# Performance work log

Measured on AMD Instinct MI355X. Metric: run time of the kernel, lower is better.

The kernel has to match this reference:

```python
import jax, jax.numpy as jnp
import numpy as np

FCM_ITERS = 3
FCM_M = 2.0
EPS = 1e-8


def batched_index_select(x, idx):
    # x: [B, C, M, 1], idx: [B, N, K] -> [B, C, N, K]
    xt = x[..., 0]  # [B, C, M]
    return jnp.take_along_axis(xt[:, :, None, :], idx[:, None, :, :], axis=3)


def fcm_centroids(x, num_clusters):
    # Fuzzy c-means soft clustering (HyperedgeConstruction).
    # x: [B, C, N, 1] -> centroids [B, C, K], weights [B, N, 1, K]
    xt = jnp.transpose(x[..., 0], (0, 2, 1))  # [B, N, C]
    B, N, C = xt.shape
    init_idx = jnp.linspace(0, N - 1, num_clusters).astype(jnp.int32)
    cent = xt[:, init_idx, :]  # [B, K, C] deterministic init
    expo = -1.0 / (FCM_M - 1.0)

    def memberships(cent):
        xn = jnp.sum(xt * xt, axis=-1)            # [B, N]
        cn = jnp.sum(cent * cent, axis=-1)        # [B, K]
        d2 = xn[:, :, None] + cn[:, None, :] - 2.0 * jnp.einsum('bnc,bkc->bnk', xt, cent)
        d2 = jnp.maximum(d2, EPS)
        inv = d2 ** expo
        return inv / jnp.sum(inv, axis=-1, keepdims=True)  # [B, N, K]

    for _ in range(FCM_ITERS):
        u = memberships(cent)
        um = u ** FCM_M
        cent = jnp.einsum('bnk,bnc->bkc', um, xt) / (jnp.sum(um, axis=1)[..., None] + EPS)
    u = memberships(cent)
    centroids = jnp.transpose(cent, (0, 2, 1))  # [B, C, K]
    return centroids, u[:, :, None, :]          # weights [B, N, 1, K]


def setup_inputs() -> dict:
    key = jax.random.key(0)
    k1, k2, k3, k4 = jax.random.split(key, 4)
    B, C, N, K = 4, 64, 8192, 16
    OC = 64
    return {
        "x": jax.random.normal(k1, (B, C, N, 1), jnp.float32),
        "edge_index": jax.random.randint(k2, (2, B, N, K), 0, N),
        "W": jax.random.normal(k3, (OC, 3 * C), jnp.float32) / np.sqrt(3 * C).astype(np.float32),
        "b": jax.random.normal(k4, (OC,), jnp.float32) * 0.01,
        "num_clusters": 50,
        "top_clusters": 5,
    }


def reference(x, edge_index, W, b, num_clusters, top_clusters):
    B, C, N, _ = x.shape
    # max-relative neighbor feature
    x_i = batched_index_select(x, edge_index[1])          # [B, C, N, K]
    x_j = batched_index_select(x, edge_index[0])          # [B, C, N, K]
    x_j = jnp.max(x_j - x_i, axis=-1, keepdims=True)      # [B, C, N, 1]
    # soft-cluster (hyperedge) feature
    centroids, weights = fcm_centroids(x, num_clusters)   # [B,C,K], [B,N,1,K]
    weights = weights[:, :, 0, :]                         # squeeze(-2) -> [B, N, K]
    _, nn_idx_centroid = jax.lax.top_k(weights, top_clusters)  # [B, N, top]
    x_j_cluster = batched_index_select(centroids[..., None], nn_idx_centroid)  # [B, C, N, top]
    # x gathered at center_idx == x broadcast over top dim
    x_j_cluster = jnp.max(x_j_cluster - x, axis=-1, keepdims=True)  # [B, C, N, 1]
    # interleaved concat: [B, C, 3, N, 1] -> [B, 3C, N, 1]
    feat = jnp.stack([x, x_j, x_j_cluster], axis=2).reshape(B, 3 * C, N, 1)
    # BasicConv: 1x1 conv + ReLU
    out = jnp.einsum('oc,bcni->boni', W, feat) + b[None, :, None, None]
    return jax.nn.relu(out)
```

## Files before the change

### kernel.cpp

```cpp
#include <hip/hip_runtime.h>


constexpr int B  = 4;
constexpr int C  = 64;
constexpr int N  = 8192;
constexpr int KE = 16;
constexpr int OC = 64;
constexpr int NC = 50;
constexpr int TC = 5;
constexpr int C3 = 192;
constexpr int NCP = 52;
constexpr int KG  = 5;
constexpr int NKG = 10;
constexpr int NS  = 8;
constexpr int MW  = 16;
constexpr float FEPS = 1e-8f;

__global__ __launch_bounds__(256) void k_transpose(const float* __restrict__ x,
                                                   float* __restrict__ xt,
                                                   float* __restrict__ xn) {
  __shared__ float tile[64][65];
  int b  = blockIdx.x >> 7;
  int n0 = (blockIdx.x & 127) << 6;
  int tid = threadIdx.x;
  int nl = tid & 63, cq = tid >> 6;
#pragma unroll
  for (int r = 0; r < 16; ++r) {
    int cc = r * 4 + cq;
    tile[cc][nl] = x[((size_t)b * C + cc) * N + n0 + nl];
  }
  __syncthreads();
  int cl = tid & 63, nq = tid >> 6;
#pragma unroll
  for (int r = 0; r < 16; ++r) {
    int nr = r * 4 + nq;
    xt[((size_t)b * N + n0 + nr) * C + cl] = tile[cl][nr];
  }
  if (tid < 64) {
    float s = 0.f;
#pragma unroll
    for (int cc = 0; cc < 64; ++cc) { float v = tile[cc][tid]; s = fmaf(v, v, s); }
    xn[(size_t)b * N + n0 + tid] = s;
  }
}

__global__ __launch_bounds__(256) void k_init(const float* __restrict__ xt,
                                              float* __restrict__ cent,
                                              float* __restrict__ cn) {
  int i = blockIdx.x * 256 + threadIdx.x;
  int lane = threadIdx.x & 63;
  int ccol = i & 63;
  int row  = i >> 6;
  int k = row % NC, b = row / NC;
  int src = (k * (N - 1)) / (NC - 1);
  float v = xt[((size_t)b * N + src) * C + ccol];
  cent[i] = v;
  float sq = v * v;
#pragma unroll
  for (int off = 32; off; off >>= 1) sq += __shfl_down(sq, off, 64);
  if (lane == 0) cn[row] = sq;
}

__global__ __launch_bounds__(512) void k_m1(const float* __restrict__ xt,
                                            const float* __restrict__ xn,
                                            const float* __restrict__ cent,
                                            const float* __restrict__ cn,
                                            float* __restrict__ um) {
  int gid = blockIdx.x;
  int xcd = gid & 7;
  int b = xcd >> 1;
  int chunk = ((gid >> 3) << 1) + (xcd & 1);
  int n0 = chunk << 6;
  int w = __builtin_amdgcn_readfirstlane((int)threadIdx.x >> 6);
  int lane = threadIdx.x & 63;
  int n = n0 + lane;
  int base = (w < 2) ? 7 * w : 14 + 6 * (w - 2);
  int cnt  = (w < 2) ? 7 : 6;
  const float* xr = xt + ((size_t)b * N + n) * C;
  const float* cb = cent + b * NC * C;
  float dot[7];
#pragma unroll
  for (int j = 0; j < 7; ++j) dot[j] = 0.f;
  for (int c4 = 0; c4 < C; c4 += 4) {
    float4 xv = *(const float4*)(xr + c4);
#pragma unroll
    for (int j = 0; j < 7; ++j) {
      int kk = base + j; kk = (kk < NC) ? kk : 0;
      float4 cv = *(const float4*)(cb + kk * C + c4);
      dot[j] = fmaf(xv.x, cv.x, dot[j]);
      dot[j] = fmaf(xv.y, cv.y, dot[j]);
      dot[j] = fmaf(xv.z, cv.z, dot[j]);
      dot[j] = fmaf(xv.w, cv.w, dot[j]);
    }
  }
  float xnv = xn[(size_t)b * N + n];
  const float* cnb = cn + b * NC;
  float inv[7];
  float psum = 0.f;
#pragma unroll
  for (int j = 0; j < 7; ++j) {
    int kk = base + j; kk = (kk < NC) ? kk : 0;
    float d2 = fmaf(-2.f, dot[j], xnv + cnb[kk]);
    d2 = fmaxf(d2, FEPS);
    float iv = 1.f / d2;
    inv[j] = iv;
    psum += (j < cnt) ? iv : 0.f;
  }
  __shared__ float s_ps[8][64];
  s_ps[w][lane] = psum;
  __syncthreads();
  float ssum = 0.f;
#pragma unroll
  for (int ww = 0; ww < 8; ++ww) ssum += s_ps[ww][lane];
  float s2i = 1.f / (ssum * ssum);
  float* up = um + ((size_t)b * N + n) * NCP + base;
#pragma unroll
  for (int j = 0; j < 7; ++j)
    if (j < cnt) up[j] = inv[j] * inv[j] * s2i;
}

__global__ __launch_bounds__(1024) void k_m2(const float* __restrict__ um,
                                             const float* __restrict__ xt,
                                             float* __restrict__ part_c,
                                             float* __restrict__ part_u) {
  int gid = blockIdx.x;
  int xcd = gid & 7;
  int b = xcd >> 1;
  int r = ((gid >> 3) << 1) + (xcd & 1);
  int kg = r >> 3;
  int s  = r & 7;
  int k0 = kg * KG;
  int w = __builtin_amdgcn_readfirstlane((int)threadIdx.x >> 6);
  int c = threadIdx.x & 63;
  int n0 = s * (N / NS);
  const float* umb = um + ((size_t)b * N + n0) * NCP + k0;
  const float* xb  = xt + ((size_t)b * N + n0) * C + c;
  float acc[KG], ua[KG];
#pragma unroll
  for (int j = 0; j < KG; ++j) { acc[j] = 0.f; ua[j] = 0.f; }
#pragma unroll 4
  for (int n = w; n < N / NS; n += MW) {
    float xv = xb[(size_t)n * C];
    const float* up = umb + (size_t)n * NCP;
#pragma unroll
    for (int j = 0; j < KG; ++j) {
      float u = up[j];
      acc[j] = fmaf(u, xv, acc[j]);
      ua[j] += u;
    }
  }
  __shared__ float s_acc[MW][KG][64];
  __shared__ float s_ua[MW][KG];
#pragma unroll
  for (int j = 0; j < KG; ++j) s_acc[w][j][c] = acc[j];
  if (c == 0) {
#pragma unroll
    for (int j = 0; j < KG; ++j) s_ua[w][j] = ua[j];
  }
  __syncthreads();
  if (w == 0) {
#pragma unroll
    for (int j = 0; j < KG; ++j) {
      float t = 0.f;
#pragma unroll
      for (int ww = 0; ww < MW; ++ww) t += s_acc[ww][j][c];
      part_c[((size_t)s * (B * NC) + b * NC + k0 + j) * C + c] = t;
    }
    if (c == 0) {
#pragma unroll
      for (int j = 0; j < KG; ++j) {
        float t = 0.f;
#pragma unroll
        for (int ww = 0; ww < MW; ++ww) t += s_ua[ww][j];
        part_u[(size_t)s * (B * NC) + b * NC + k0 + j] = t;
      }
    }
  }
}

__global__ __launch_bounds__(256) void k_m3(const float* __restrict__ part_c,
                                            const float* __restrict__ part_u,
                                            float* __restrict__ cent,
                                            float* __restrict__ cn) {
  int i = blockIdx.x * 256 + threadIdx.x;
  int lane = threadIdx.x & 63;
  int row = i >> 6;
  float tot = 0.f;
#pragma unroll
  for (int s = 0; s < NS; ++s) tot += part_c[(size_t)s * (B * NC * C) + i];
  float us = 0.f;
#pragma unroll
  for (int s = 0; s < NS; ++s) us += part_u[(size_t)s * (B * NC) + row];
  float v = tot / (us + FEPS);
  cent[i] = v;
  float sq = v * v;
#pragma unroll
  for (int off = 32; off; off >>= 1) sq += __shfl_down(sq, off, 64);
  if (lane == 0) cn[row] = sq;
}

__global__ __launch_bounds__(512) void k_top5(const float* __restrict__ xt,
                                              const float* __restrict__ xn,
                                              const float* __restrict__ cent,
                                              const float* __restrict__ cn,
                                              int* __restrict__ t5) {
  int gid = blockIdx.x;
  int xcd = gid & 7;
  int b = xcd >> 1;
  int chunk = ((gid >> 3) << 1) + (xcd & 1);
  int n0 = chunk << 6;
  int w = __builtin_amdgcn_readfirstlane((int)threadIdx.x >> 6);
  int lane = threadIdx.x & 63;
  int n = n0 + lane;
  int base = (w < 2) ? 7 * w : 14 + 6 * (w - 2);
  int cnt  = (w < 2) ? 7 : 6;
  const float* xr = xt + ((size_t)b * N + n) * C;
  const float* cb = cent + b * NC * C;
  float dot[7];
#pragma unroll
  for (int j = 0; j < 7; ++j) dot[j] = 0.f;
  for (int c4 = 0; c4 < C; c4 += 4) {
    float4 xv = *(const float4*)(xr + c4);
#pragma unroll
    for (int j = 0; j < 7; ++j) {
      int kk = base + j; kk = (kk < NC) ? kk : 0;
      float4 cv = *(const float4*)(cb + kk * C + c4);
      dot[j] = fmaf(xv.x, cv.x, dot[j]);
      dot[j] = fmaf(xv.y, cv.y, dot[j]);
      dot[j] = fmaf(xv.z, cv.z, dot[j]);
      dot[j] = fmaf(xv.w, cv.w, dot[j]);
    }
  }
  float xnv = xn[(size_t)b * N + n];
  const float* cnb = cn + b * NC;
  __shared__ float s_inv[NC][65];
#pragma unroll
  for (int j = 0; j < 7; ++j) {
    int kk = base + j; kk = (kk < NC) ? kk : 0;
    float d2 = fmaxf(fmaf(-2.f, dot[j], xnv + cnb[kk]), FEPS);
    float iv = 1.f / d2;
    if (j < cnt) s_inv[base + j][lane] = iv;
  }
  __syncthreads();
  if (w == 0) {
    float v[NC];
#pragma unroll
    for (int k = 0; k < NC; ++k) v[k] = s_inv[k][lane];
    unsigned long long taken = 0ull;
    int* tp = t5 + ((size_t)b * N + n) * TC;
#pragma unroll
    for (int t = 0; t < TC; ++t) {
      float best = -1.f;
      int bi = 0;
#pragma unroll
      for (int k = 0; k < NC; ++k) {
        bool ok = (((taken >> k) & 1ull) == 0ull) && (v[k] > best);
        best = ok ? v[k] : best;
        bi   = ok ? k : bi;
      }
      taken |= (1ull << bi);
      tp[t] = bi;
    }
  }
}

__global__ __launch_bounds__(512, 4) void k_out(const float* __restrict__ xt,
                                                const float* __restrict__ cent,
                                                const float* __restrict__ W,
                                                const int* __restrict__ t5,
                                                const int* __restrict__ eidx,
                                                const float* __restrict__ bias,
                                                float* __restrict__ out) {
  __shared__ float s_w[OC][C3 + 2];
  int tid = threadIdx.x;
  for (int i = tid; i < OC * C3; i += 512) {
    int o = i / C3, cc = i - o * C3;
    s_w[o][cc] = W[i];
  }
  __syncthreads();
  int gid = blockIdx.x;
  int xcd = gid & 7;
  int b = xcd >> 1;
  int chunk = ((gid >> 3) << 1) + (xcd & 1);
  int wv = __builtin_amdgcn_readfirstlane(tid >> 6);
  int lane = tid & 63;
  int n0 = chunk * 64 + wv * 8;
  const float* xtb = xt + ((size_t)b * N) * C;
  const float* cb  = cent + b * NC * C;
  const int* e0b = eidx + ((size_t)b * N) * KE;
  const int* e1b = eidx + ((size_t)(B + b) * N) * KE;
  int c = lane;
  float fA[8], fB[8], fC[8];
#pragma unroll
  for (int j = 0; j < 8; ++j) {
    int n = n0 + j;
    const int* p0 = e0b + (size_t)n * KE;
    const int* p1 = e1b + (size_t)n * KE;
    const int* tp = t5 + ((size_t)b * N + n) * TC;
    float x0 = xtb[(size_t)n * C + c];
    float g0[KE], g1[KE];
#pragma unroll
    for (int k = 0; k < KE; ++k) {
      g0[k] = xtb[(size_t)p0[k] * C + c];
      g1[k] = xtb[(size_t)p1[k] * C + c];
    }
    float cv[TC];
#pragma unroll
    for (int t = 0; t < TC; ++t) cv[t] = cb[(size_t)tp[t] * C + c];
    float m1 = g0[0] - g1[0];
#pragma unroll
    for (int k = 1; k < KE; ++k) m1 = fmaxf(m1, g0[k] - g1[k]);
    float cm = cv[0];
#pragma unroll
    for (int t = 1; t < TC; ++t) cm = fmaxf(cm, cv[t]);
    fA[j] = x0; fB[j] = m1; fC[j] = cm - x0;
  }
  float bo = bias[lane];
  float acc[8];
#pragma unroll
  for (int j = 0; j < 8; ++j) acc[j] = bo;
  for (int cp = 0; cp < 64; ++cp) {
    float w0 = s_w[lane][3 * cp + 0];
    float w1 = s_w[lane][3 * cp + 1];
    float w2 = s_w[lane][3 * cp + 2];
#pragma unroll
    for (int j = 0; j < 8; ++j) {
      float a0 = __uint_as_float(__builtin_amdgcn_readlane(__float_as_uint(fA[j]), cp));
      float a1 = __uint_as_float(__builtin_amdgcn_readlane(__float_as_uint(fB[j]), cp));
      float a2 = __uint_as_float(__builtin_amdgcn_readlane(__float_as_uint(fC[j]), cp));
      acc[j] = fmaf(w0, a0, acc[j]);
      acc[j] = fmaf(w1, a1, acc[j]);
      acc[j] = fmaf(w2, a2, acc[j]);
    }
  }
  float* op = out + ((size_t)b * OC + lane) * N + n0;
  *(float4*)(op)     = make_float4(fmaxf(acc[0], 0.f), fmaxf(acc[1], 0.f),
                                   fmaxf(acc[2], 0.f), fmaxf(acc[3], 0.f));
  *(float4*)(op + 4) = make_float4(fmaxf(acc[4], 0.f), fmaxf(acc[5], 0.f),
                                   fmaxf(acc[6], 0.f), fmaxf(acc[7], 0.f));
}

extern "C" void kernel_launch(void* const* d_in, const int* in_sizes, int n_in,
                              void* d_out, int out_size, void* d_ws, size_t ws_size,
                              hipStream_t stream) {
  const float* x    = (const float*)d_in[0];
  const int*   eidx = (const int*)d_in[1];
  const float* W    = (const float*)d_in[2];
  const float* bias = (const float*)d_in[3];

  float* ws   = (float*)d_ws;
  float* xt   = ws;
  float* xn   = xt + (size_t)B * N * C;
  float* cent = xn + (size_t)B * N;
  float* cn   = cent + B * NC * C;
  float* um   = cn + 256;
  float* pc   = um + (size_t)B * N * NCP;
  float* pu   = pc + (size_t)NS * B * NC * C;
  int*   t5   = (int*)(pu + NS * B * NC);
  float* out  = (float*)d_out;

  k_transpose<<<dim3(B * (N / 64)), dim3(256), 0, stream>>>(x, xt, xn);
  k_init<<<dim3((B * NC * C) / 256), dim3(256), 0, stream>>>(xt, cent, cn);
  for (int it = 0; it < 3; ++it) {
    k_m1<<<dim3(512), dim3(512), 0, stream>>>(xt, xn, cent, cn, um);
    k_m2<<<dim3(B * NKG * NS), dim3(1024), 0, stream>>>(um, xt, pc, pu);
    k_m3<<<dim3((B * NC * C) / 256), dim3(256), 0, stream>>>(pc, pu, cent, cn);
  }
  k_top5<<<dim3(512), dim3(512), 0, stream>>>(xt, xn, cent, cn, t5);
  k_out<<<dim3(512), dim3(512), 0, stream>>>(xt, cent, W, t5, eidx, bias, out);
}
```

Before: 228.4 us.

## Transpose membership buffer to cluster-major and restage conv features through LDS

The membership weights are now stored cluster-major ([B,NC,N]) instead of point-major with padding. k_m1 writes coalesced rows per cluster, and k_m2 gives each wave a contiguous 64-point span that it reads with float4 loads instead of strided scalar loads. k_out no longer stages W in LDS or broadcasts features with readlane. Each block writes its 192x64 feature tile to LDS, and each wave computes 8 output channels for 64 points, reading W directly from global memory (wave-uniform, likely scalar loads). Output stores are now contiguous per channel, at the cost of an extra barrier and changed LDS usage.

```diff
diff --git a/kernel.cpp b/kernel.cpp
--- a/kernel.cpp
+++ b/kernel.cpp
@@ -9,7 +9,6 @@
 constexpr int NC = 50;
 constexpr int TC = 5;
 constexpr int C3 = 192;
-constexpr int NCP = 52;
 constexpr int KG  = 5;
 constexpr int NKG = 10;
 constexpr int NS  = 8;
@@ -65,7 +64,7 @@
                                             const float* __restrict__ xn,
                                             const float* __restrict__ cent,
                                             const float* __restrict__ cn,
-                                            float* __restrict__ um) {
+                                            float* __restrict__ umT) {
   int gid = blockIdx.x;
   int xcd = gid & 7;
   int b = xcd >> 1;
@@ -113,13 +112,13 @@
 #pragma unroll
   for (int ww = 0; ww < 8; ++ww) ssum += s_ps[ww][lane];
   float s2i = 1.f / (ssum * ssum);
-  float* up = um + ((size_t)b * N + n) * NCP + base;
+  float* upT = umT + ((size_t)b * NC + base) * N + n;
 #pragma unroll
   for (int j = 0; j < 7; ++j)
-    if (j < cnt) up[j] = inv[j] * inv[j] * s2i;
-}
-
-__global__ __launch_bounds__(1024) void k_m2(const float* __restrict__ um,
+    if (j < cnt) upT[(size_t)j * N] = inv[j] * inv[j] * s2i;
+}
+
+__global__ __launch_bounds__(1024) void k_m2(const float* __restrict__ umT,
                                              const float* __restrict__ xt,
                                              float* __restrict__ part_c,
                                              float* __restrict__ part_u) {
@@ -132,21 +131,27 @@
   int k0 = kg * KG;
   int w = __builtin_amdgcn_readfirstlane((int)threadIdx.x >> 6);
   int c = threadIdx.x & 63;
-  int n0 = s * (N / NS);
-  const float* umb = um + ((size_t)b * N + n0) * NCP + k0;
-  const float* xb  = xt + ((size_t)b * N + n0) * C + c;
+  int sn0 = s * (N / NS);
+  int nb = w * 64;
+  const float* uT = umT + ((size_t)b * NC + k0) * N + sn0 + nb;
+  const float* xb = xt + ((size_t)(b * N + sn0 + nb)) * C + c;
   float acc[KG], ua[KG];
 #pragma unroll
   for (int j = 0; j < KG; ++j) { acc[j] = 0.f; ua[j] = 0.f; }
-#pragma unroll 4
-  for (int n = w; n < N / NS; n += MW) {
-    float xv = xb[(size_t)n * C];
-    const float* up = umb + (size_t)n * NCP;
-#pragma unroll
-    for (int j = 0; j < KG; ++j) {
-      float u = up[j];
-      acc[j] = fmaf(u, xv, acc[j]);
-      ua[j] += u;
+  for (int n4 = 0; n4 < 64; n4 += 4) {
+    float4 u4[KG];
+#pragma unroll
+    for (int j = 0; j < KG; ++j)
+      u4[j] = *(const float4*)(uT + (size_t)j * N + n4);
+#pragma unroll
+    for (int t = 0; t < 4; ++t) {
+      float xv = xb[(size_t)(n4 + t) * C];
+#pragma unroll
+      for (int j = 0; j < KG; ++j) {
+        float u = (t == 0) ? u4[j].x : (t == 1) ? u4[j].y : (t == 2) ? u4[j].z : u4[j].w;
+        acc[j] = fmaf(u, xv, acc[j]);
+        ua[j] += u;
+      }
     }
   }
   __shared__ float s_acc[MW][KG][64];
@@ -271,29 +276,25 @@
                                                 const int* __restrict__ eidx,
                                                 const float* __restrict__ bias,
                                                 float* __restrict__ out) {
-  __shared__ float s_w[OC][C3 + 2];
+  __shared__ float s_feat[C3][65];
   int tid = threadIdx.x;
-  for (int i = tid; i < OC * C3; i += 512) {
-    int o = i / C3, cc = i - o * C3;
-    s_w[o][cc] = W[i];
-  }
-  __syncthreads();
   int gid = blockIdx.x;
   int xcd = gid & 7;
   int b = xcd >> 1;
   int chunk = ((gid >> 3) << 1) + (xcd & 1);
   int wv = __builtin_amdgcn_readfirstlane(tid >> 6);
   int lane = tid & 63;
-  int n0 = chunk * 64 + wv * 8;
+  int n0 = chunk * 64;
+  int nw0 = n0 + wv * 8;
   const float* xtb = xt + ((size_t)b * N) * C;
   const float* cb  = cent + b * NC * C;
   const int* e0b = eidx + ((size_t)b * N) * KE;
   const int* e1b = eidx + ((size_t)(B + b) * N) * KE;
   int c = lane;
-  float fA[8], fB[8], fC[8];
+  int fr = wv * 8;
 #pragma unroll
   for (int j = 0; j < 8; ++j) {
-    int n = n0 + j;
+    int n = nw0 + j;
     const int* p0 = e0b + (size_t)n * KE;
     const int* p1 = e1b + (size_t)n * KE;
     const int* tp = t5 + ((size_t)b * N + n) * TC;
@@ -313,31 +314,26 @@
     float cm = cv[0];
 #pragma unroll
     for (int t = 1; t < TC; ++t) cm = fmaxf(cm, cv[t]);
-    fA[j] = x0; fB[j] = m1; fC[j] = cm - x0;
-  }
-  float bo = bias[lane];
+    s_feat[3 * c + 0][fr + j] = x0;
+    s_feat[3 * c + 1][fr + j] = m1;
+    s_feat[3 * c + 2][fr + j] = cm - x0;
+  }
+  __syncthreads();
+  int o0 = wv * 8;
   float acc[8];
 #pragma unroll
-  for (int j = 0; j < 8; ++j) acc[j] = bo;
-  for (int cp = 0; cp < 64; ++cp) {
-    float w0 = s_w[lane][3 * cp + 0];
-    float w1 = s_w[lane][3 * cp + 1];
-    float w2 = s_w[lane][3 * cp + 2];
-#pragma unroll
-    for (int j = 0; j < 8; ++j) {
-      float a0 = __uint_as_float(__builtin_amdgcn_readlane(__float_as_uint(fA[j]), cp));
-      float a1 = __uint_as_float(__builtin_amdgcn_readlane(__float_as_uint(fB[j]), cp));
-      float a2 = __uint_as_float(__builtin_amdgcn_readlane(__float_as_uint(fC[j]), cp));
-      acc[j] = fmaf(w0, a0, acc[j]);
-      acc[j] = fmaf(w1, a1, acc[j]);
-      acc[j] = fmaf(w2, a2, acc[j]);
-    }
-  }
-  float* op = out + ((size_t)b * OC + lane) * N + n0;
-  *(float4*)(op)     = make_float4(fmaxf(acc[0], 0.f), fmaxf(acc[1], 0.f),
-                                   fmaxf(acc[2], 0.f), fmaxf(acc[3], 0.f));
-  *(float4*)(op + 4) = make_float4(fmaxf(acc[4], 0.f), fmaxf(acc[5], 0.f),
-                                   fmaxf(acc[6], 0.f), fmaxf(acc[7], 0.f));
+  for (int oj = 0; oj < 8; ++oj) acc[oj] = bias[o0 + oj];
+#pragma unroll 4
+  for (int f = 0; f < C3; ++f) {
+    float v = s_feat[f][lane];
+#pragma unroll
+    for (int oj = 0; oj < 8; ++oj)
+      acc[oj] = fmaf(W[(size_t)(o0 + oj) * C3 + f], v, acc[oj]);
+  }
+  float* ob = out + ((size_t)b * OC + o0) * N + n0 + lane;
+#pragma unroll
+  for (int oj = 0; oj < 8; ++oj)
+    ob[(size_t)oj * N] = fmaxf(acc[oj], 0.f);
 }
 
 extern "C" void kernel_launch(void* const* d_in, const int* in_sizes, int n_in,
@@ -353,8 +349,8 @@
   float* xn   = xt + (size_t)B * N * C;
   float* cent = xn + (size_t)B * N;
   float* cn   = cent + B * NC * C;
-  float* um   = cn + 256;
-  float* pc   = um + (size_t)B * N * NCP;
+  float* umT  = cn + 256;
+  float* pc   = umT + (size_t)B * NC * N;
   float* pu   = pc + (size_t)NS * B * NC * C;
   int*   t5   = (int*)(pu + NS * B * NC);
   float* out  = (float*)d_out;
@@ -362,8 +358,8 @@
   k_transpose<<<dim3(B * (N / 64)), dim3(256), 0, stream>>>(x, xt, xn);
   k_init<<<dim3((B * NC * C) / 256), dim3(256), 0, stream>>>(xt, cent, cn);
   for (int it = 0; it < 3; ++it) {
-    k_m1<<<dim3(512), dim3(512), 0, stream>>>(xt, xn, cent, cn, um);
-    k_m2<<<dim3(B * NKG * NS), dim3(1024), 0, stream>>>(um, xt, pc, pu);
+    k_m1<<<dim3(512), dim3(512), 0, stream>>>(xt, xn, cent, cn, umT);
+    k_m2<<<dim3(B * NKG * NS), dim3(1024), 0, stream>>>(umT, xt, pc, pu);
     k_m3<<<dim3((B * NC * C) / 256), dim3(256), 0, stream>>>(pc, pu, cent, cn);
   }
   k_top5<<<dim3(512), dim3(512), 0, stream>>>(xt, xn, cent, cn, t5);
```

New measurement: 240.9 us. 1.05x slower.
